# Kernel optimization log

Measured on AMD Instinct MI355X. Metric: run time of the kernel, lower is better.

Reference implementation:

```python
import jax, jax.numpy as jnp
import numpy as np

B, H, W, D, K = 64, 32, 32, 128, 1024


def setup_inputs() -> dict:
    key = jax.random.key(0)
    k1, k2 = jax.random.split(key)
    z_e = jax.random.normal(k1, (B, H, W, D), dtype=jnp.float32)
    # GlorotUniform over (k, d): limit = sqrt(6 / (k + d))
    limit = float(np.sqrt(6.0 / (K + D)))
    codebook = jax.random.uniform(k2, (K, D), dtype=jnp.float32, minval=-limit, maxval=limit)
    return {"z_e": z_e, "codebook": codebook}


def reference(z_e, codebook):
    # Original: norm = ||z_e[..., None, :] - codebook||_2 over d, then argmin over k.
    # Squared distance has the same argmin; expand to avoid the (B,H,W,k,d) tensor:
    # ||z - c||^2 = ||z||^2 - 2 z.c + ||c||^2
    z2 = jnp.sum(z_e * z_e, axis=-1, keepdims=True)           # (B,H,W,1)
    c2 = jnp.sum(codebook * codebook, axis=-1)                # (k,)
    dots = jnp.einsum('bhwd,kd->bhwk', z_e, codebook)         # (B,H,W,k)
    dist2 = z2 - 2.0 * dots + c2                              # (B,H,W,k)
    q_z = jnp.argmin(dist2, axis=-1)                          # (B,H,W) int
    return q_z
```

## Files before the change

### kernel.cpp

```cpp
#include <hip/hip_runtime.h>
#include <stdint.h>

#define NPTS   65536
#define DDIM   128
#define KCODES 1024

typedef __attribute__((ext_vector_type(8))) _Float16  half8;
typedef __attribute__((ext_vector_type(4))) float     f32x4;
typedef __attribute__((ext_vector_type(4))) int       int4v;
typedef __attribute__((ext_vector_type(2))) _Float16  half2v;

__device__ __forceinline__ void split16(float x, _Float16& hi, _Float16& lo) {
  _Float16 h = (__builtin_fabsf(x) < 6.103515625e-05f) ? (_Float16)0.f : (_Float16)x;
  hi = h;
  lo = (_Float16)(__fmul_rn(__fsub_rn(x, (float)h), 2048.f));
}

__device__ __forceinline__ float np_sumsq_128(const float* __restrict__ row) {
  float r[8];
#pragma unroll
  for (int k = 0; k < 8; ++k) r[k] = __fmul_rn(row[k], row[k]);
  for (int i = 8; i < 128; i += 8)
#pragma unroll
    for (int k = 0; k < 8; ++k) r[k] = __fadd_rn(r[k], __fmul_rn(row[i + k], row[i + k]));
  float s01 = __fadd_rn(r[0], r[1]), s23 = __fadd_rn(r[2], r[3]);
  float s45 = __fadd_rn(r[4], r[5]), s67 = __fadd_rn(r[6], r[7]);
  return __fadd_rn(__fadd_rn(s01, s23), __fadd_rn(s45, s67));
}

__device__ __forceinline__ void async_copy16(const void* g, void* l) {
  auto gp = (const __attribute__((address_space(1))) unsigned int*)(uintptr_t)g;
  auto lp = (__attribute__((address_space(3))) unsigned int*)(unsigned)(uintptr_t)l;
  __builtin_amdgcn_global_load_lds(gp, lp, 16, 0, 0);
}

constexpr size_t SZ_B   = (size_t)KCODES * DDIM * 2;
constexpr size_t OFF_B1 = 0;
constexpr size_t OFF_B2 = SZ_B;
constexpr size_t OFF_C2 = 2 * SZ_B;
constexpr size_t WS_NEED = OFF_C2 + (size_t)KCODES * 4;

__global__ __launch_bounds__(256) void vq_prep_cb(const float* __restrict__ cb,
                                                  _Float16* __restrict__ B1,
                                                  _Float16* __restrict__ B2,
                                                  float* __restrict__ c2) {
  const int w = threadIdx.x >> 6, ln = threadIdx.x & 63;
  const int code = blockIdx.x * 4 + w;
  const float2 cv = ((const float2*)(cb + (size_t)code * DDIM))[ln];
  _Float16 h0, l0, h1, l1;
  split16(cv.x, h0, l0); split16(cv.y, h1, l1);
  const int kg = ln >> 2;
  const int o  = 2 * (ln & 3);
  const size_t dst = (size_t)code * DDIM + (size_t)((kg ^ (code & 15)) * 8 + o);
  *(half2v*)(B1 + dst) = (half2v){h0, h1};
  *(half2v*)(B2 + dst) = (half2v){l0, l1};

  if (threadIdx.x < 32) {
    const int cc = blockIdx.x * 4 + (threadIdx.x >> 3), jj = threadIdx.x & 7;
    const float* row = cb + (size_t)cc * DDIM;
    float e = row[jj];
    float acc = __fmul_rn(e, e);
    for (int i = 1; i < 16; ++i) {
      e = row[i * 8 + jj];
      acc = __fadd_rn(acc, __fmul_rn(e, e));
    }
    float a1 = __fadd_rn(acc, __shfl_xor(acc, 1));
    float a2 = __fadd_rn(a1, __shfl_xor(a1, 2));
    float a4 = __fadd_rn(a2, __shfl_xor(a2, 4));
    if (jj == 0) c2[cc] = a4;
  }
}

__global__ __launch_bounds__(256, 2) void vq_gemm(
    const float* __restrict__ z,
    const unsigned short* __restrict__ B1g, const unsigned short* __restrict__ B2g,
    const float* __restrict__ c2g, int* __restrict__ out) {
  __shared__ alignas(16) char smem[16384 + 16384 + 4096 + 512];
  unsigned short* Bs1 = (unsigned short*)smem;
  unsigned short* Bs2 = (unsigned short*)(smem + 16384);
  float* c2sh = (float*)(smem + 32768);
  float* z2sh = (float*)(smem + 32768 + 4096);
  float* Ls   = (float*)smem;

  const int tid = threadIdx.x;
  const int ln = tid & 63, wr = tid >> 6;
  const int l15 = ln & 15, q = ln >> 4;
  const size_t row0 = (size_t)blockIdx.x * 128;
  const float4* z4 = (const float4*)z;

  for (int cc = 0; cc < 4; ++cc) {
#pragma unroll
    for (int j = 0; j < 4; ++j) {
      const int idx = tid + j * 256;
      float4 v = z4[(row0 + cc * 32) * 32 + idx];
      *(float4*)&Ls[(idx >> 5) * 132 + (idx & 31) * 4] = v;
    }
    __syncthreads();
    {
      const int r = tid >> 3, jj = tid & 7;
      const float* row = &Ls[r * 132];
      float e = row[jj];
      float acc = __fmul_rn(e, e);
      for (int i = 1; i < 16; ++i) {
        e = row[i * 8 + jj];
        acc = __fadd_rn(acc, __fmul_rn(e, e));
      }
      float a1 = __fadd_rn(acc, __shfl_xor(acc, 1));
      float a2 = __fadd_rn(a1, __shfl_xor(a1, 2));
      float a4 = __fadd_rn(a2, __shfl_xor(a2, 4));
      if (jj == 0) z2sh[cc * 32 + r] = a4;
    }
    __syncthreads();
  }

#pragma unroll
  for (int j = 0; j < 4; ++j) {
    const int s = tid + j * 256;
    async_copy16(B2g + s * 8, Bs2 + s * 8);
    async_copy16(B1g + s * 8, Bs1 + s * 8);
  }
  async_copy16(c2g + tid * 4, c2sh + tid * 4);

  half8 a1f[2][4], a2f[2][4];
#pragma unroll
  for (int rf = 0; rf < 2; ++rf) {
    const float* zr = z + (row0 + wr * 32 + rf * 16 + l15) * DDIM;
#pragma unroll
    for (int ks = 0; ks < 4; ++ks) {
      float tmp[8];
      *(float4*)tmp       = *(const float4*)(zr + ks * 32 + q * 8);
      *(float4*)(tmp + 4) = *(const float4*)(zr + ks * 32 + q * 8 + 4);
      half8 h, l;
#pragma unroll
      for (int e = 0; e < 8; ++e) {
        _Float16 hh, ll;
        split16(tmp[e], hh, ll);
        h[e] = hh; l[e] = ll;
      }
      a1f[rf][ks] = h; a2f[rf][ks] = l;
    }
  }

  float mv[8];
  int mi[8];
#pragma unroll
  for (int i = 0; i < 8; ++i) { mv[i] = 3.0e38f; mi[i] = 0; }

  __syncthreads();

  float z2r[8];
#pragma unroll
  for (int rf = 0; rf < 2; ++rf)
#pragma unroll
    for (int reg = 0; reg < 4; ++reg)
      z2r[rf * 4 + reg] = z2sh[wr * 32 + rf * 16 + q * 4 + reg];

  for (int iter = 0; iter < 16; ++iter) {
    const int c0 = iter * 64;
    f32x4 acc[2][4];
#pragma unroll
    for (int rf = 0; rf < 2; ++rf)
#pragma unroll
      for (int cf = 0; cf < 4; ++cf) acc[rf][cf] = (f32x4){0.f, 0.f, 0.f, 0.f};

#pragma unroll
    for (int ks = 0; ks < 4; ++ks) {
      half8 b[4];
#pragma unroll
      for (int cf = 0; cf < 4; ++cf)
        b[cf] = *(const half8*)&Bs2[(cf * 16 + l15) * 128 + (((ks * 4 + q) ^ l15) * 8)];
#pragma unroll
      for (int rf = 0; rf < 2; ++rf)
#pragma unroll
        for (int cf = 0; cf < 4; ++cf)
          acc[rf][cf] = __builtin_amdgcn_mfma_f32_16x16x32_f16(a1f[rf][ks], b[cf],
                                                               acc[rf][cf], 0, 0, 0);
    }

    __syncthreads();
    if (iter < 15) {
#pragma unroll
      for (int j = 0; j < 4; ++j) {
        const int s = tid + j * 256;
        async_copy16(B2g + (size_t)(c0 + 64) * DDIM + s * 8, Bs2 + s * 8);
      }
    }

#pragma unroll
    for (int ks = 0; ks < 4; ++ks) {
      half8 b[4];
#pragma unroll
      for (int cf = 0; cf < 4; ++cf)
        b[cf] = *(const half8*)&Bs1[(cf * 16 + l15) * 128 + (((ks * 4 + q) ^ l15) * 8)];
#pragma unroll
      for (int rf = 0; rf < 2; ++rf)
#pragma unroll
        for (int cf = 0; cf < 4; ++cf)
          acc[rf][cf] = __builtin_amdgcn_mfma_f32_16x16x32_f16(a2f[rf][ks], b[cf],
                                                               acc[rf][cf], 0, 0, 0);
    }
#pragma unroll
    for (int rf = 0; rf < 2; ++rf)
#pragma unroll
      for (int cf = 0; cf < 4; ++cf) acc[rf][cf] = acc[rf][cf] * 4.8828125e-4f;

#pragma unroll
    for (int ks = 0; ks < 4; ++ks) {
      half8 b[4];
#pragma unroll
      for (int cf = 0; cf < 4; ++cf)
        b[cf] = *(const half8*)&Bs1[(cf * 16 + l15) * 128 + (((ks * 4 + q) ^ l15) * 8)];
#pragma unroll
      for (int rf = 0; rf < 2; ++rf)
#pragma unroll
        for (int cf = 0; cf < 4; ++cf)
          acc[rf][cf] = __builtin_amdgcn_mfma_f32_16x16x32_f16(a1f[rf][ks], b[cf],
                                                               acc[rf][cf], 0, 0, 0);
    }

#pragma unroll
    for (int rf = 0; rf < 2; ++rf)
#pragma unroll
      for (int reg = 0; reg < 4; ++reg) {
        const int slot = rf * 4 + reg;
        const float z2v = z2r[slot];
#pragma unroll
        for (int cf = 0; cf < 4; ++cf) {
          const float c2v = c2sh[c0 + cf * 16 + l15];
          float dot = acc[rf][cf][reg];
          float v = __fadd_rn(__fsub_rn(z2v, __fmul_rn(2.f, dot)), c2v);
          int idx = c0 + cf * 16 + l15;
          if (v < mv[slot]) { mv[slot] = v; mi[slot] = idx; }
        }
      }

    __syncthreads();
    if (iter < 15) {
#pragma unroll
      for (int j = 0; j < 4; ++j) {
        const int s = tid + j * 256;
        async_copy16(B1g + (size_t)(c0 + 64) * DDIM + s * 8, Bs1 + s * 8);
      }
    }
  }

#pragma unroll
  for (int slot = 0; slot < 8; ++slot) {
    float v = mv[slot];
    int i = mi[slot];
#pragma unroll
    for (int m = 1; m <= 8; m <<= 1) {
      float ov = __shfl_xor(v, m);
      int oi = __shfl_xor(i, m);
      if (ov < v || (ov == v && oi < i)) { v = ov; i = oi; }
    }
    mv[slot] = v; mi[slot] = i;
  }

  if (l15 == 0) {
#pragma unroll
    for (int rf = 0; rf < 2; ++rf) {
      int4v r = {mi[rf * 4 + 0], mi[rf * 4 + 1], mi[rf * 4 + 2], mi[rf * 4 + 3]};
      *(int4v*)&out[row0 + wr * 32 + rf * 16 + q * 4] = r;
    }
  }
}

__global__ __launch_bounds__(256) void vq_fallback(const float* __restrict__ z,
                                                   const float* __restrict__ cb,
                                                   int* __restrict__ out) {
  __shared__ float zs[DDIM];
  __shared__ float z2s;
  __shared__ float bv[256];
  __shared__ int bi[256];
  const int p = blockIdx.x, tid = threadIdx.x;
  if (tid < DDIM) zs[tid] = z[(size_t)p * DDIM + tid];
  __syncthreads();
  if (tid == 0) z2s = np_sumsq_128(zs);
  __syncthreads();
  const float z2p = z2s;
  float best = 3.0e38f;
  int bidx = 0;
  for (int c = tid; c < KCODES; c += 256) {
    const float* cr = cb + (size_t)c * DDIM;
    double acc = 0.0;
#pragma unroll 8
    for (int d = 0; d < DDIM; ++d) acc += (double)zs[d] * (double)cr[d];
    float dfl = (float)acc;
    float c2k = np_sumsq_128(cr);
    float v = __fadd_rn(__fsub_rn(z2p, __fmul_rn(2.f, dfl)), c2k);
    if (v < best) { best = v; bidx = c; }
  }
  bv[tid] = best; bi[tid] = bidx;
  __syncthreads();
  for (int off = 128; off > 0; off >>= 1) {
    if (tid < off) {
      if (bv[tid + off] < bv[tid] || (bv[tid + off] == bv[tid] && bi[tid + off] < bi[tid])) {
        bv[tid] = bv[tid + off]; bi[tid] = bi[tid + off];
      }
    }
    __syncthreads();
  }
  if (tid == 0) out[p] = bi[0];
}

extern "C" void kernel_launch(void* const* d_in, const int* in_sizes, int n_in,
                              void* d_out, int out_size, void* d_ws, size_t ws_size,
                              hipStream_t stream) {
  (void)in_sizes; (void)n_in; (void)out_size;
  const float* z = (const float*)d_in[0];
  const float* cb = (const float*)d_in[1];
  int* out = (int*)d_out;

  if (d_ws != nullptr && ws_size >= WS_NEED) {
    char* ws = (char*)d_ws;
    _Float16* B1 = (_Float16*)(ws + OFF_B1);
    _Float16* B2 = (_Float16*)(ws + OFF_B2);
    float* c2 = (float*)(ws + OFF_C2);

    vq_prep_cb<<<KCODES / 4, 256, 0, stream>>>(cb, B1, B2, c2);
    vq_gemm<<<NPTS / 128, 256, 0, stream>>>(
        z, (const unsigned short*)(ws + OFF_B1), (const unsigned short*)(ws + OFF_B2),
        c2, out);
  } else {
    vq_fallback<<<NPTS, 256, 0, stream>>>(z, cb, out);
  }
}
```

Baseline: 118.5 us.

## Double-buffer codebook tiles in LDS and prefetch next tile at loop start

Replaces the single Bs1/Bs2 LDS buffers with two ping-pong 32 KB buffers, each holding both the hi and lo codebook halves. The next tile is prefetched asynchronously at the top of each iteration, and one of the two barriers per iteration is dropped. The aim is to hide global-to-LDS latency behind the MFMA work and cut synchronisation stalls. LDS use per block roughly doubles, which may limit occupancy, and correctness depends on the async copies being complete by the end-of-loop barrier.

```diff
diff --git a/kernel.cpp b/kernel.cpp
--- a/kernel.cpp
+++ b/kernel.cpp
@@ -75,11 +75,9 @@
     const float* __restrict__ z,
     const unsigned short* __restrict__ B1g, const unsigned short* __restrict__ B2g,
     const float* __restrict__ c2g, int* __restrict__ out) {
-  __shared__ alignas(16) char smem[16384 + 16384 + 4096 + 512];
-  unsigned short* Bs1 = (unsigned short*)smem;
-  unsigned short* Bs2 = (unsigned short*)(smem + 16384);
-  float* c2sh = (float*)(smem + 32768);
-  float* z2sh = (float*)(smem + 32768 + 4096);
+  __shared__ alignas(16) char smem[32768 * 2 + 4096 + 512];
+  float* c2sh = (float*)(smem + 65536);
+  float* z2sh = (float*)(smem + 65536 + 4096);
   float* Ls   = (float*)smem;
 
   const int tid = threadIdx.x;
@@ -113,13 +111,16 @@
     __syncthreads();
   }
 
-#pragma unroll
-  for (int j = 0; j < 4; ++j) {
-    const int s = tid + j * 256;
-    async_copy16(B2g + s * 8, Bs2 + s * 8);
-    async_copy16(B1g + s * 8, Bs1 + s * 8);
-  }
-  async_copy16(c2g + tid * 4, c2sh + tid * 4);
+  {
+    unsigned short* b0 = (unsigned short*)smem;
+#pragma unroll
+    for (int j = 0; j < 4; ++j) {
+      const int s = tid + j * 256;
+      async_copy16(B2g + s * 8, b0 + s * 8);
+      async_copy16(B1g + s * 8, b0 + 8192 + s * 8);
+    }
+    async_copy16(c2g + tid * 4, c2sh + tid * 4);
+  }
 
   half8 a1f[2][4], a2f[2][4];
 #pragma unroll
@@ -155,8 +156,23 @@
     for (int reg = 0; reg < 4; ++reg)
       z2r[rf * 4 + reg] = z2sh[wr * 32 + rf * 16 + q * 4 + reg];
 
-  for (int iter = 0; iter < 16; ++iter) {
-    const int c0 = iter * 64;
+  for (int u = 0; u < 16; ++u) {
+    const unsigned short* cur = (const unsigned short*)(smem + (u & 1) * 32768);
+    const unsigned short* bs2 = cur;
+    const unsigned short* bs1 = cur + 8192;
+    const int c0 = u * 64;
+
+    if (u < 15) {
+      unsigned short* nb = (unsigned short*)(smem + ((u + 1) & 1) * 32768);
+      const size_t goff = (size_t)(u + 1) * 8192;
+#pragma unroll
+      for (int j = 0; j < 4; ++j) {
+        const int s = tid + j * 256;
+        async_copy16(B2g + goff + s * 8, nb + s * 8);
+        async_copy16(B1g + goff + s * 8, nb + 8192 + s * 8);
+      }
+    }
+
     f32x4 acc[2][4];
 #pragma unroll
     for (int rf = 0; rf < 2; ++rf)
@@ -168,7 +184,7 @@
       half8 b[4];
 #pragma unroll
       for (int cf = 0; cf < 4; ++cf)
-        b[cf] = *(const half8*)&Bs2[(cf * 16 + l15) * 128 + (((ks * 4 + q) ^ l15) * 8)];
+        b[cf] = *(const half8*)&bs2[(cf * 16 + l15) * 128 + (((ks * 4 + q) ^ l15) * 8)];
 #pragma unroll
       for (int rf = 0; rf < 2; ++rf)
 #pragma unroll
@@ -177,21 +193,12 @@
                                                                acc[rf][cf], 0, 0, 0);
     }
 
-    __syncthreads();
-    if (iter < 15) {
-#pragma unroll
-      for (int j = 0; j < 4; ++j) {
-        const int s = tid + j * 256;
-        async_copy16(B2g + (size_t)(c0 + 64) * DDIM + s * 8, Bs2 + s * 8);
-      }
-    }
-
 #pragma unroll
     for (int ks = 0; ks < 4; ++ks) {
       half8 b[4];
 #pragma unroll
       for (int cf = 0; cf < 4; ++cf)
-        b[cf] = *(const half8*)&Bs1[(cf * 16 + l15) * 128 + (((ks * 4 + q) ^ l15) * 8)];
+        b[cf] = *(const half8*)&bs1[(cf * 16 + l15) * 128 + (((ks * 4 + q) ^ l15) * 8)];
 #pragma unroll
       for (int rf = 0; rf < 2; ++rf)
 #pragma unroll
@@ -209,7 +216,7 @@
       half8 b[4];
 #pragma unroll
       for (int cf = 0; cf < 4; ++cf)
-        b[cf] = *(const half8*)&Bs1[(cf * 16 + l15) * 128 + (((ks * 4 + q) ^ l15) * 8)];
+        b[cf] = *(const half8*)&bs1[(cf * 16 + l15) * 128 + (((ks * 4 + q) ^ l15) * 8)];
 #pragma unroll
       for (int rf = 0; rf < 2; ++rf)
 #pragma unroll
@@ -235,13 +242,6 @@
       }
 
     __syncthreads();
-    if (iter < 15) {
-#pragma unroll
-      for (int j = 0; j < 4; ++j) {
-        const int s = tid + j * 256;
-        async_copy16(B1g + (size_t)(c0 + 64) * DDIM + s * 8, Bs1 + s * 8);
-      }
-    }
   }
 
 #pragma unroll
```

Measured after the change: 121.4 us. 1.02x slower.
